# Optimization experiments

Hardware: AMD Instinct MI355X
Metric: run time of the kernel (lower is better)

## Reference

```python
import jax, jax.numpy as jnp
import numpy as np

N_ATOMS = 16384
B_GRAPHS = 64
K_CLUSTERS = 64          # clusters per molecule
M_CLUSTERS = B_GRAPHS * K_CLUSTERS
HID = 256                # hidden_channels (== node_attr feature dim)
FIL = 256                # num_filters
ECH = 64                 # edge_channels (num gaussians)
L_INT = 6                # num_interactions
CUTOFF = 10.0
LN2 = float(np.log(2.0))


def _ssp(x):
    # ShiftedSoftplus
    return jax.nn.softplus(x) - LN2


def setup_inputs() -> dict:
    key = jax.random.key(0)
    ks = jax.random.split(key, 12)
    pos = jax.random.normal(ks[0], (N_ATOMS, 3), jnp.float32) * 2.0
    node_attr = jax.random.normal(ks[1], (N_ATOMS, HID), jnp.float32)
    atoms_per_cluster = N_ATOMS // M_CLUSTERS
    subgraph_index = (jnp.arange(N_ATOMS) // atoms_per_cluster).astype(jnp.int64)
    batch = (jnp.arange(N_ATOMS) // (N_ATOMS // B_GRAPHS)).astype(jnp.int64)
    s = 0.05
    params = {
        "mlp_w1": jax.random.normal(ks[2], (L_INT, ECH, FIL), jnp.float32) * s,
        "mlp_b1": jnp.zeros((L_INT, FIL), jnp.float32),
        "mlp_w2": jax.random.normal(ks[3], (L_INT, FIL, FIL), jnp.float32) * s,
        "mlp_b2": jnp.zeros((L_INT, FIL), jnp.float32),
        "lin1_w": jax.random.normal(ks[4], (L_INT, HID, FIL), jnp.float32) * s,  # no bias
        "lin2_w": jax.random.normal(ks[5], (L_INT, FIL, HID), jnp.float32) * s,
        "lin2_b": jnp.zeros((L_INT, HID), jnp.float32),
        "lin_w":  jax.random.normal(ks[6], (L_INT, HID, HID), jnp.float32) * s,
        "lin_b":  jnp.zeros((L_INT, HID), jnp.float32),
    }
    return {"pos": pos, "node_attr": node_attr,
            "subgraph_index": subgraph_index, "batch": batch,
            "num_graphs": B_GRAPHS, "clusters_per_graph": K_CLUSTERS, **params}


def _complete_graph_edges(num_graphs, clusters_per_graph):
    # static (numpy) construction of per-molecule complete graph, no self loops
    K = clusters_per_graph
    i = np.arange(K)
    pr, pc = np.meshgrid(i, i, indexing='ij')
    m = pr != pc
    pr, pc = pr[m], pc[m]                       # (K*(K-1),)
    off = np.arange(num_graphs)[:, None] * K    # (B,1)
    row = jnp.asarray((off + pr[None, :]).reshape(-1))
    col = jnp.asarray((off + pc[None, :]).reshape(-1))
    return row, col


def reference(pos, node_attr, subgraph_index, batch, num_graphs, clusters_per_graph,
              mlp_w1, mlp_b1, mlp_w2, mlp_b2, lin1_w, lin2_w, lin2_b, lin_w, lin_b):
    M = num_graphs * clusters_per_graph
    # ---- coarse_grain: scatter-mean atoms into clusters ----
    cnt = jax.ops.segment_sum(jnp.ones((pos.shape[0],), pos.dtype), subgraph_index, num_segments=M)
    cnt = jnp.maximum(cnt, 1.0)[:, None]
    cluster_pos = jax.ops.segment_sum(pos, subgraph_index, num_segments=M) / cnt        # (M,3)
    cluster_attr = jax.ops.segment_sum(node_attr, subgraph_index, num_segments=M) / cnt  # (M,H)

    # ---- complete graph per molecule ----
    row, col = _complete_graph_edges(num_graphs, clusters_per_graph)
    edge_length = jnp.linalg.norm(cluster_pos[row] - cluster_pos[col], axis=1)          # (E,)

    # ---- GaussianSmearing ----
    offset = jnp.linspace(0.0, CUTOFF, ECH)
    coeff = -0.5 / (offset[1] - offset[0]) ** 2
    edge_attr = jnp.exp(coeff * (edge_length[:, None] - offset[None, :]) ** 2)          # (E,ECH)

    # smooth cutoff envelope
    C = 0.5 * (jnp.cos(edge_length * jnp.pi / CUTOFF) + 1.0)
    C = C * (edge_length <= CUTOFF).astype(C.dtype)                                     # (E,)

    # ---- SchNetEncoder (embed_node=False) ----
    h = cluster_attr
    for l in range(L_INT):
        # filter-generating MLP
        W = _ssp(edge_attr @ mlp_w1[l] + mlp_b1[l]) @ mlp_w2[l] + mlp_b2[l]             # (E,F)
        W = W * C[:, None]
        x = h @ lin1_w[l]                                                               # (M,F)
        agg = jax.ops.segment_sum(x[row] * W, col, num_segments=M)                      # (M,F)
        x = agg @ lin2_w[l] + lin2_b[l]                                                 # (M,H)
        x = _ssp(x)
        x = x @ lin_w[l] + lin_b[l]
        h = h + x                                                                       # residual
    return h
```

## Files before the change

### kernel.cpp

```cpp
#include <hip/hip_runtime.h>
#include <cstdint>

#define NATOMS 16384
#define BGRAPH 64
#define KC     64
#define MCL    (BGRAPH*KC)
#define HIDC   256
#define FILC   256
#define ECHC   64
#define LINT   6

#define TGRID  1024
#define TROWS  1088
#define NBP    1056

typedef __bf16 bf16x8 __attribute__((ext_vector_type(8)));
typedef __bf16 bf16x2 __attribute__((ext_vector_type(2)));
typedef float  f32x4  __attribute__((ext_vector_type(4)));
typedef unsigned short u16x8 __attribute__((ext_vector_type(8)));

__device__ __forceinline__ float bf2f(unsigned short u) {
    unsigned int x = ((unsigned int)u) << 16;
    return __builtin_bit_cast(float, x);
}
__device__ __forceinline__ unsigned short f2bf(float f) {
    __bf16 h = (__bf16)f;
    return __builtin_bit_cast(unsigned short, h);
}
__device__ __forceinline__ unsigned int pk2(float a, float b) {
    bf16x2 v = { (__bf16)a, (__bf16)b };
    return __builtin_bit_cast(unsigned int, v);
}
__device__ __forceinline__ float ssp_poly(float x) {
    float u = fminf(x * x, 4.0f);
    float q = u * fmaf(u, fmaf(u, 3.4722222e-4f, -5.2083333e-3f), 0.125f);
    return fmaf(0.5f, x, q);
}
__device__ __forceinline__ float ssp_fast(float x) {
    float m = fmaxf(x, 0.0f);
    float t = __builtin_amdgcn_exp2f(-fabsf(x) * 1.44269504088896341f);
    float l = __builtin_amdgcn_logf(1.0f + t);
    return fmaf(0.69314718055994531f, l, m - 0.69314718055994531f);
}
__device__ __forceinline__ int sw_off(int row, int col) {
    int s = (row + (row >> 3)) & 7;
    return row * 256 + ((((col >> 3) ^ s) << 3) | (col & 7));
}
__device__ __forceinline__ int phi_sw(int row) {
    return ((row & 7) ^ ((row >> 3) & 7)) & 7;
}

#define CGB   1024
#define N_W1  (LINT*16384)
#define N_BIG (LINT*65536)
#define PACK_BLOCKS ((N_W1 + 4*N_BIG + 255)/256)
__global__ void k_prep(const float* __restrict__ pos, const float* __restrict__ attr,
                       const int* __restrict__ subi,
                       float* __restrict__ h, unsigned short* __restrict__ h_bf,
                       float* __restrict__ cpos,
                       const float* __restrict__ w1_src, const float* __restrict__ w2_src,
                       const float* __restrict__ l1_src, const float* __restrict__ l2_src,
                       const float* __restrict__ lw_src,
                       unsigned short* __restrict__ w1p, unsigned short* __restrict__ w2p,
                       unsigned short* __restrict__ l1p, unsigned short* __restrict__ l2p,
                       unsigned short* __restrict__ lwp)
{
    if (blockIdx.x >= CGB) {
        int idx = (blockIdx.x - CGB) * 256 + threadIdx.x;
        if (idx < N_W1) {
            int j = idx & 7, lane = (idx >> 3) & 63, kt = (idx >> 9) & 1;
            int mt = (idx >> 10) & 15, l = idx >> 14;
            int ech = kt*32 + (lane >> 4)*8 + j;
            int f1  = mt*16 + (lane & 15);
            w1p[idx] = f2bf(w1_src[(l*64 + ech)*256 + f1]);
            return;
        }
        int r = idx - N_W1;
        int which = r / N_BIG;
        if (which >= 4) return;
        int e = r - which * N_BIG;
        const float* src = (which == 0) ? w2_src : (which == 1) ? l1_src
                         : (which == 2) ? l2_src : lw_src;
        unsigned short* dst = (which == 0) ? w2p : (which == 1) ? l1p
                            : (which == 2) ? l2p : lwp;
        int n = e % 256;
        int k = (e / 256) % 256;
        int l = e / 65536;
        int nt = n >> 4, kt = k >> 5, q = (k >> 3) & 3, j = k & 7;
        int lane = q*16 + (n & 15);
        dst[l*65536 + ((nt*8 + kt)*64 + lane)*8 + j] = f2bf(src[e]);
        return;
    }
    const int m = blockIdx.x * 4 + (threadIdx.x >> 6);
    const int lane = threadIdx.x & 63;
    const bool is64 = (subi[8] == 1);
    int lo = 0, hi = NATOMS;
    while (lo < hi) { int mid = (lo + hi) >> 1;
        int v = is64 ? subi[2*mid] : subi[mid];
        if (v < m) lo = mid + 1; else hi = mid; }
    int lo2 = lo, hi2 = NATOMS;
    while (lo2 < hi2) { int mid = (lo2 + hi2) >> 1;
        int v = is64 ? subi[2*mid] : subi[mid];
        if (v < m + 1) lo2 = mid + 1; else hi2 = mid; }
    const int cnt2 = lo2 - lo;
    const float inv = 1.0f / (float)(cnt2 > 0 ? cnt2 : 1);

    float4 s = {0.f, 0.f, 0.f, 0.f};
    for (int a = lo; a < lo2; a++) {
        const float4 v = *reinterpret_cast<const float4*>(&attr[a*HIDC + lane*4]);
        s.x += v.x; s.y += v.y; s.z += v.z; s.w += v.w;
    }
    s.x *= inv; s.y *= inv; s.z *= inv; s.w *= inv;
    *reinterpret_cast<float4*>(&h[m*HIDC + lane*4]) = s;
    const int o = m*HIDC + lane*4;
    h_bf[o+0] = f2bf(s.x); h_bf[o+1] = f2bf(s.y);
    h_bf[o+2] = f2bf(s.z); h_bf[o+3] = f2bf(s.w);
    if (lane < 3) {
        float p = 0.f;
        for (int a = lo; a < lo2; a++) p += pos[a*3 + lane];
        cpos[m*3 + lane] = p * inv;
    }
}

#define OSTR 264
__global__ __launch_bounds__(512, 6) void k_tab(
    const unsigned short* __restrict__ w1p_all, const unsigned short* __restrict__ w2p_all,
    const float* __restrict__ b1_all, const float* __restrict__ b2_all,
    unsigned short* __restrict__ table)
{
    __shared__ unsigned short G_s[64 * 256];
    __shared__ unsigned short phi_s[16 * OSTR];
    __shared__ float C_s[64];
    __shared__ float d_s[64];

    const int l  = blockIdx.x / 17;
    const int g0 = (blockIdx.x % 17) * 64;
    const unsigned short* w1p = w1p_all + (size_t)l*16384;
    const unsigned short* w2p = w2p_all + (size_t)l*65536;
    const float* b1 = b1_all + l*256;
    const float* b2 = b2_all + l*256;

    const int t  = threadIdx.x;
    const int w  = t >> 6, lane = t & 63;
    const int quad = lane >> 4, l16 = lane & 15;

    if (t < 64) {
        float d = (float)(g0 + t) * 0.009765625f;
        d_s[t] = d;
        float Cv = 0.5f * (__cosf(d * 0.31415926535897932f) + 1.0f);
        C_s[t] = (d <= 10.0f) ? Cv : 0.0f;
    }
    __syncthreads();

    const float DELTA = 10.0f / 63.0f;
    const float C2 = (-0.5f / (DELTA * DELTA)) * 1.44269504088896341f;
    {
        float d = d_s[lane];
        u16x8 ph;
        #pragma unroll
        for (int j = 0; j < 8; j++) {
            float diff = d - (float)(w*8 + j) * DELTA;
            ph[j] = f2bf(__builtin_amdgcn_exp2f(C2 * diff * diff));
        }
        *reinterpret_cast<u16x8*>(&phi_s[lane*64 + ((w ^ phi_sw(lane)) << 3)]) = ph;
    }
    __syncthreads();

    f32x4 acc1[2][4];
    #pragma unroll
    for (int mt = 0; mt < 2; mt++) {
        const int f1b = (w*2 + mt)*16 + quad*4;
        float4 bq = *reinterpret_cast<const float4*>(&b1[f1b]);
        #pragma unroll
        for (int nt = 0; nt < 4; nt++) {
            acc1[mt][nt][0] = bq.x; acc1[mt][nt][1] = bq.y;
            acc1[mt][nt][2] = bq.z; acc1[mt][nt][3] = bq.w;
        }
    }
    #pragma unroll
    for (int kt = 0; kt < 2; kt++) {
        bf16x8 bfr[4];
        #pragma unroll
        for (int nt = 0; nt < 4; nt++) {
            int row = nt*16 + l16;
            bfr[nt] = *reinterpret_cast<const bf16x8*>(
                &phi_s[row*64 + (((kt*4 + quad) ^ phi_sw(row)) << 3)]);
        }
        #pragma unroll
        for (int mt = 0; mt < 2; mt++) {
            bf16x8 afr = *reinterpret_cast<const bf16x8*>(
                w1p + (((w*2 + mt)*2 + kt)*64 + lane)*8);
            #pragma unroll
            for (int nt = 0; nt < 4; nt++)
                acc1[mt][nt] = __builtin_amdgcn_mfma_f32_16x16x32_bf16(afr, bfr[nt], acc1[mt][nt], 0, 0, 0);
        }
    }

    float Cn[4];
    #pragma unroll
    for (int nt = 0; nt < 4; nt++) Cn[nt] = C_s[nt*16 + l16];

    #pragma unroll
    for (int mt = 0; mt < 2; mt++) {
        const int f1b = (w*2 + mt)*16 + quad*4;
        #pragma unroll
        for (int nt = 0; nt < 4; nt++) {
            float v0 = ssp_poly(acc1[mt][nt][0]) * Cn[nt];
            float v1 = ssp_poly(acc1[mt][nt][1]) * Cn[nt];
            float v2 = ssp_poly(acc1[mt][nt][2]) * Cn[nt];
            float v3 = ssp_poly(acc1[mt][nt][3]) * Cn[nt];
            uint2 pp;
            pp.x = pk2(v0, v1);
            pp.y = pk2(v2, v3);
            int edge = nt*16 + l16;
            int s = (edge + (edge >> 3)) & 7;
            int a = edge*256 + ((((f1b >> 3) ^ s) << 3) | (f1b & 7));
            *reinterpret_cast<uint2*>(&G_s[a]) = pp;
        }
    }
    __syncthreads();

    f32x4 acc2[4][2];
    #pragma unroll
    for (int a = 0; a < 4; a++)
        #pragma unroll
        for (int bb = 0; bb < 2; bb++) acc2[a][bb] = f32x4{0.f,0.f,0.f,0.f};

    #pragma unroll
    for (int kt = 0; kt < 8; kt++) {
        bf16x8 afr[4];
        #pragma unroll
        for (int mt = 0; mt < 4; mt++) {
            int row = mt*16 + l16;
            int s = (row + (row >> 3)) & 7;
            afr[mt] = *reinterpret_cast<const bf16x8*>(&G_s[row*256 + (((kt*4 + quad) ^ s) << 3)]);
        }
        #pragma unroll
        for (int nt = 0; nt < 2; nt++) {
            const int ntg = w*2 + nt;
            bf16x8 bfr = *reinterpret_cast<const bf16x8*>(w2p + ((ntg*8 + kt)*64 + lane)*8);
            #pragma unroll
            for (int mt = 0; mt < 4; mt++)
                acc2[mt][nt] = __builtin_amdgcn_mfma_f32_16x16x32_bf16(afr[mt], bfr, acc2[mt][nt], 0, 0, 0);
        }
    }

    #pragma unroll
    for (int nt = 0; nt < 2; nt++) {
        const int f = (w*2 + nt)*16 + l16;
        const float b2v = b2[f];
        #pragma unroll
        for (int mt = 0; mt < 4; mt++) {
            #pragma unroll
            for (int i = 0; i < 4; i++) {
                int e = mt*16 + quad*4 + i;
                table[((size_t)l*TROWS + g0 + e)*256 + f] =
                    f2bf(fmaf(C_s[e], b2v, acc2[mt][nt][i]));
            }
        }
    }
}

__device__ __forceinline__ void gemm16(const unsigned short* A_s, const unsigned short* Bp,
                                       int w, int lane, f32x4 acc[4])
{
    const int quad = lane >> 4, l16 = lane & 15;
    const int s = (l16 + (l16 >> 3)) & 7;
    #pragma unroll
    for (int nt = 0; nt < 4; nt++) acc[nt] = f32x4{0.f,0.f,0.f,0.f};
    #pragma unroll
    for (int kt = 0; kt < 8; kt++) {
        bf16x8 afr = *reinterpret_cast<const bf16x8*>(&A_s[l16*256 + (((kt*4 + quad) ^ s) << 3)]);
        #pragma unroll
        for (int nt = 0; nt < 4; nt++) {
            bf16x8 bfr = *reinterpret_cast<const bf16x8*>(Bp + (((w*4 + nt)*8 + kt)*64 + lane)*8);
            acc[nt] = __builtin_amdgcn_mfma_f32_16x16x32_bf16(afr, bfr, acc[nt], 0, 0, 0);
        }
    }
}
__device__ __forceinline__ void gemm16w16(const unsigned short* A_s, const unsigned short* Bp,
                                          int w, int lane, f32x4& acc)
{
    const int quad = lane >> 4, l16 = lane & 15;
    const int s = (l16 + (l16 >> 3)) & 7;
    acc = f32x4{0.f,0.f,0.f,0.f};
    #pragma unroll
    for (int kt = 0; kt < 8; kt++) {
        bf16x8 afr = *reinterpret_cast<const bf16x8*>(&A_s[l16*256 + (((kt*4 + quad) ^ s) << 3)]);
        bf16x8 bfr = *reinterpret_cast<const bf16x8*>(Bp + (((w*8 + kt)*64 + lane))*8);
        acc = __builtin_amdgcn_mfma_f32_16x16x32_bf16(afr, bfr, acc, 0, 0, 0);
    }
}

#define PK_TOTAL (LINT*NBP*64)
#define PK_BLOCKS ((PK_TOTAL + 255)/256)
__global__ __launch_bounds__(256) void k_gemm0p(
    const unsigned short* __restrict__ A_bf, const unsigned short* __restrict__ Bp,
    unsigned short* __restrict__ out_bf,
    const unsigned short* __restrict__ table, unsigned short* __restrict__ tbl2)
{
    if (blockIdx.x >= 256) {
        int idx = (blockIdx.x - 256) * 256 + threadIdx.x;
        if (idx >= PK_TOTAL) return;
        int fc2 = idx & 63;
        int qq = idx >> 6;
        int bin = qq % NBP;
        int l = qq / NBP;
        if (bin > TGRID) return;
        const unsigned short* Ts = table + ((size_t)l*TROWS + bin)*256 + fc2*4;
        ushort4 a = *reinterpret_cast<const ushort4*>(Ts);
        ushort4 b = *reinterpret_cast<const ushort4*>(Ts + 256);
        ushort4 d;
        d.x = f2bf(bf2f(b.x) - bf2f(a.x));
        d.y = f2bf(bf2f(b.y) - bf2f(a.y));
        d.z = f2bf(bf2f(b.z) - bf2f(a.z));
        d.w = f2bf(bf2f(b.w) - bf2f(a.w));
        unsigned short* dst = tbl2 + ((size_t)l*NBP + bin)*512 + fc2*8;
        *reinterpret_cast<ushort4*>(dst)     = a;
        *reinterpret_cast<ushort4*>(dst + 4) = d;
        return;
    }
    __shared__ unsigned short A_s[16 * 256];
    const int mb = blockIdx.x;
    const int t = threadIdx.x;
    const int w = t >> 6, lane = t & 63, quad = lane >> 4, l16 = lane & 15;

    {
        int r = t >> 4, seg = t & 15;
        int s = (r + (r >> 3)) & 7;
        const u16x8* src = reinterpret_cast<const u16x8*>(A_bf + (size_t)(mb*16 + r)*256 + seg*16);
        int c = seg*2;
        *reinterpret_cast<u16x8*>(&A_s[r*256 + (((c  ) ^ s) << 3)]) = src[0];
        *reinterpret_cast<u16x8*>(&A_s[r*256 + (((c+1) ^ s) << 3)]) = src[1];
    }
    __syncthreads();

    f32x4 acc[4];
    gemm16(A_s, Bp, w, lane, acc);

    #pragma unroll
    for (int nt = 0; nt < 4; nt++)
        #pragma unroll
        for (int i = 0; i < 4; i++) {
            int rg = mb*16 + quad*4 + i;
            int col = w*64 + nt*16 + l16;
            out_bf[(size_t)rg*256 + col] = f2bf(acc[nt][i]);
        }
}

template<int DO_X>
__global__ __launch_bounds__(1024) void k_layer(
    const float* __restrict__ cpos,
    const unsigned short* __restrict__ xin, unsigned short* __restrict__ xout,
    const unsigned short* __restrict__ Tp,
    const unsigned short* __restrict__ lin2p, const float* __restrict__ lin2_b,
    const unsigned short* __restrict__ linp,  const float* __restrict__ lin_b,
    const unsigned short* __restrict__ lin1p,
    float* __restrict__ h)
{
    __shared__ unsigned short x_s[64 * 256];
    __shared__ unsigned short A0[16 * 256];
    __shared__ unsigned short A1[16 * 256];
    __shared__ int   idx_s[1024];
    __shared__ float frac_s[1024];

    const int blk = blockIdx.x;
    const int b = blk >> 2, q = blk & 3;
    const int t = threadIdx.x;
    const int w = t >> 6, lane = t & 63, quad = lane >> 4, l16 = lane & 15;

    {
        int r = t >> 4, seg = t & 15;
        const u16x8* s8 = reinterpret_cast<const u16x8*>(
            xin + ((size_t)(b*64 + r))*256 + seg*16);
        u16x8* dst = reinterpret_cast<u16x8*>(&x_s[r*256 + seg*16]);
        dst[0] = s8[0]; dst[1] = s8[1];
    }
    {
        int r = t >> 4, cc = t & 15;
        int gr = b*64 + r, gc = b*64 + q*16 + cc;
        float ax = cpos[gr*3 + 0] - cpos[gc*3 + 0];
        float ay = cpos[gr*3 + 1] - cpos[gc*3 + 1];
        float az = cpos[gr*3 + 2] - cpos[gc*3 + 2];
        float d = sqrtf(ax*ax + ay*ay + az*az);
        int i; float fr;
        if (gr == gc || d >= 10.0f) { i = TGRID; fr = 0.0f; }
        else {
            float u = d * 102.4f;
            i = (int)u; fr = u - (float)i;
        }
        idx_s[t] = i * 512; frac_s[t] = fr;
    }
    __syncthreads();

    {
        const int c   = t >> 6;
        const int fc2 = t & 63;
        float a4[4] = {0.f, 0.f, 0.f, 0.f};
        #pragma unroll 8
        for (int r = 0; r < 64; r++) {
            const int   pi = __builtin_amdgcn_readfirstlane(idx_s[r*16 + c]);
            const float fr = frac_s[r*16 + c];
            const u16x8 td = *reinterpret_cast<const u16x8*>(Tp + pi + fc2*8);
            const ushort4 x4 = *reinterpret_cast<const ushort4*>(&x_s[r*256 + fc2*4]);
            float w0 = fmaf(fr, bf2f(td[4]), bf2f(td[0]));
            float w1 = fmaf(fr, bf2f(td[5]), bf2f(td[1]));
            float w2 = fmaf(fr, bf2f(td[6]), bf2f(td[2]));
            float w3 = fmaf(fr, bf2f(td[7]), bf2f(td[3]));
            a4[0] = fmaf(bf2f(x4.x), w0, a4[0]);
            a4[1] = fmaf(bf2f(x4.y), w1, a4[1]);
            a4[2] = fmaf(bf2f(x4.z), w2, a4[2]);
            a4[3] = fmaf(bf2f(x4.w), w3, a4[3]);
        }
        uint2 pv;
        pv.x = pk2(a4[0], a4[1]);
        pv.y = pk2(a4[2], a4[3]);
        int s2 = (c + (c >> 3)) & 7;
        *reinterpret_cast<uint2*>(
            &A0[c*256 + ((((fc2 >> 1) ^ s2) << 3) | ((fc2 & 1) * 4))]) = pv;
    }
    __syncthreads();

    const int col = w*16 + l16;
    const int rbase_g = b*64 + q*16;
    f32x4 acc;
    gemm16w16(A0, lin2p, w, lane, acc);
    float bv = lin2_b[col];
    #pragma unroll
    for (int i = 0; i < 4; i++)
        A1[sw_off(quad*4 + i, col)] = f2bf(ssp_fast(acc[i] + bv));
    __syncthreads();

    gemm16w16(A1, linp, w, lane, acc);
    bv = lin_b[col];
    float hv[4];
    #pragma unroll
    for (int i = 0; i < 4; i++) {
        int rg = rbase_g + quad*4 + i;
        float v = acc[i] + bv + h[(size_t)rg*256 + col];
        h[(size_t)rg*256 + col] = v;
        hv[i] = v;
    }
    if (DO_X) {
        #pragma unroll
        for (int i = 0; i < 4; i++)
            A0[sw_off(quad*4 + i, col)] = f2bf(hv[i]);
        __syncthreads();
        gemm16w16(A0, lin1p, w, lane, acc);
        #pragma unroll
        for (int i = 0; i < 4; i++) {
            int rg = rbase_g + quad*4 + i;
            xout[(size_t)rg*256 + col] = f2bf(acc[i]);
        }
    }
}

extern "C" void kernel_launch(void* const* d_in, const int* in_sizes, int n_in,
                              void* d_out, int out_size, void* d_ws, size_t ws_size,
                              hipStream_t stream)
{
    const float* pos    = (const float*)d_in[0];
    const float* nattr  = (const float*)d_in[1];
    const int*   subi   = (const int*)d_in[2];
    const float* mlp_w1 = (const float*)d_in[6];
    const float* mlp_b1 = (const float*)d_in[7];
    const float* mlp_w2 = (const float*)d_in[8];
    const float* mlp_b2 = (const float*)d_in[9];
    const float* lin1_w = (const float*)d_in[10];
    const float* lin2_w = (const float*)d_in[11];
    const float* lin2_b = (const float*)d_in[12];
    const float* lin_w  = (const float*)d_in[13];
    const float* lin_b  = (const float*)d_in[14];
    float* h = (float*)d_out;

    char* p = (char*)d_ws;
    auto alloc = [&](size_t bytes) { char* r = p; p += (bytes + 255) & ~(size_t)255; return r; };
    unsigned short* h_bf   = (unsigned short*)alloc((size_t)MCL*256*2);
    unsigned short* x0buf  = (unsigned short*)alloc((size_t)MCL*256*2);
    unsigned short* x1buf  = (unsigned short*)alloc((size_t)MCL*256*2);
    unsigned short* table  = (unsigned short*)alloc((size_t)LINT*TROWS*256*2);
    unsigned short* tbl2   = (unsigned short*)alloc((size_t)LINT*NBP*512*2);
    float*          cpos   = (float*)alloc((size_t)MCL*3*4);
    unsigned short* w1p    = (unsigned short*)alloc((size_t)LINT*16384*2);
    unsigned short* w2p    = (unsigned short*)alloc((size_t)LINT*65536*2);
    unsigned short* lin1p  = (unsigned short*)alloc((size_t)LINT*65536*2);
    unsigned short* lin2p  = (unsigned short*)alloc((size_t)LINT*65536*2);
    unsigned short* linp   = (unsigned short*)alloc((size_t)LINT*65536*2);

    k_prep<<<CGB + PACK_BLOCKS, 256, 0, stream>>>(
        pos, nattr, subi, h, h_bf, cpos,
        mlp_w1, mlp_w2, lin1_w, lin2_w, lin_w,
        w1p, w2p, lin1p, lin2p, linp);

    k_tab<<<LINT*17, 512, 0, stream>>>(w1p, w2p, mlp_b1, mlp_b2, table);

    k_gemm0p<<<256 + PK_BLOCKS, 256, 0, stream>>>(h_bf, lin1p, x0buf, table, tbl2);

    for (int l = 0; l < LINT; l++) {
        const unsigned short* xin  = (l & 1) ? x1buf : x0buf;
        unsigned short*       xout = (l & 1) ? x0buf : x1buf;
        const unsigned short* Tl = tbl2 + (size_t)l*NBP*512;
        if (l < LINT-1) {
            k_layer<1><<<BGRAPH*4, 1024, 0, stream>>>(cpos, xin, xout, Tl,
                lin2p + (size_t)l*65536, lin2_b + l*256,
                linp + (size_t)l*65536, lin_b + l*256,
                lin1p + (size_t)(l+1)*65536, h);
        } else {
            k_layer<0><<<BGRAPH*4, 1024, 0, stream>>>(cpos, xin, xout, Tl,
                lin2p + (size_t)l*65536, lin2_b + l*256,
                linp + (size_t)l*65536, lin_b + l*256,
                lin1p, h);
        }
    }
}
```

Measured before the change: 231.7 us.

## Fuse table packing and initial GEMM into k_tab; split layers into 512 blocks

The table kernel now writes the interpolation table directly in the paired layout (value plus next-bin value), and the initial lin1 GEMM runs as extra blocks of the same launch, which removes the k_gemm0p kernel and the intermediate table buffer. Each layer kernel now uses 512 blocks of 512 threads covering 8 destination clusters each, instead of 256 blocks of 1024 threads covering 16. The MFMA tiles are padded with zero rows and half of each 16-row tile is discarded, so matrix work per output row doubles in exchange for more blocks and higher occupancy. Interpolation now computes the difference on the fly from two stored values rather than reading a precomputed delta.

```diff
diff --git a/kernel.cpp b/kernel.cpp
--- a/kernel.cpp
+++ b/kernel.cpp
@@ -11,8 +11,7 @@
 #define LINT   6
 
 #define TGRID  1024
-#define TROWS  1088
-#define NBP    1056
+#define NBP    1088
 
 typedef __bf16 bf16x8 __attribute__((ext_vector_type(8)));
 typedef __bf16 bf16x2 __attribute__((ext_vector_type(2)));
@@ -122,16 +121,63 @@
     }
 }
 
-#define OSTR 264
-__global__ __launch_bounds__(512, 6) void k_tab(
+__device__ __forceinline__ void gemm16x2(const unsigned short* A_s, const unsigned short* Bp,
+                                         int w, int lane, f32x4 acc[2])
+{
+    const int quad = lane >> 4, l16 = lane & 15;
+    const int s = (l16 + (l16 >> 3)) & 7;
+    acc[0] = f32x4{0.f,0.f,0.f,0.f};
+    acc[1] = f32x4{0.f,0.f,0.f,0.f};
+    #pragma unroll
+    for (int kt = 0; kt < 8; kt++) {
+        bf16x8 afr = *reinterpret_cast<const bf16x8*>(&A_s[l16*256 + (((kt*4 + quad) ^ s) << 3)]);
+        #pragma unroll
+        for (int nt = 0; nt < 2; nt++) {
+            bf16x8 bfr = *reinterpret_cast<const bf16x8*>(Bp + (((w*2 + nt)*8 + kt)*64 + lane)*8);
+            acc[nt] = __builtin_amdgcn_mfma_f32_16x16x32_bf16(afr, bfr, acc[nt], 0, 0, 0);
+        }
+    }
+}
+
+#define NTB   (LINT*17)
+#define OSTR  264
+__global__ __launch_bounds__(512) void k_tab(
     const unsigned short* __restrict__ w1p_all, const unsigned short* __restrict__ w2p_all,
     const float* __restrict__ b1_all, const float* __restrict__ b2_all,
-    unsigned short* __restrict__ table)
+    unsigned short* __restrict__ tbl2,
+    const unsigned short* __restrict__ h_bf, const unsigned short* __restrict__ lin1p,
+    unsigned short* __restrict__ x0buf)
 {
     __shared__ unsigned short G_s[64 * 256];
     __shared__ unsigned short phi_s[16 * OSTR];
     __shared__ float C_s[64];
     __shared__ float d_s[64];
+
+    const int t  = threadIdx.x;
+    const int w  = t >> 6, lane = t & 63;
+    const int quad = lane >> 4, l16 = lane & 15;
+
+    if (blockIdx.x >= NTB) {
+        const int mb = blockIdx.x - NTB;
+        unsigned short* A_s = G_s;
+        {
+            int r = t >> 5, seg = t & 31;
+            int s = (r + (r >> 3)) & 7;
+            u16x8 v = *reinterpret_cast<const u16x8*>(h_bf + (size_t)(mb*16 + r)*256 + seg*8);
+            *reinterpret_cast<u16x8*>(&A_s[r*256 + ((seg ^ s) << 3)]) = v;
+        }
+        __syncthreads();
+        f32x4 acc[2];
+        gemm16x2(A_s, lin1p, w, lane, acc);
+        #pragma unroll
+        for (int nt = 0; nt < 2; nt++) {
+            int col = (w*2 + nt)*16 + l16;
+            #pragma unroll
+            for (int i = 0; i < 4; i++)
+                x0buf[(size_t)(mb*16 + quad*4 + i)*256 + col] = f2bf(acc[nt][i]);
+        }
+        return;
+    }
 
     const int l  = blockIdx.x / 17;
     const int g0 = (blockIdx.x % 17) * 64;
@@ -139,10 +185,6 @@
     const unsigned short* w2p = w2p_all + (size_t)l*65536;
     const float* b1 = b1_all + l*256;
     const float* b2 = b2_all + l*256;
-
-    const int t  = threadIdx.x;
-    const int w  = t >> 6, lane = t & 63;
-    const int quad = lane >> 4, l16 = lane & 15;
 
     if (t < 64) {
         float d = (float)(g0 + t) * 0.009765625f;
@@ -245,111 +287,29 @@
         }
     }
 
+    unsigned short* base = tbl2 + (size_t)l*NBP*512;
     #pragma unroll
     for (int nt = 0; nt < 2; nt++) {
         const int f = (w*2 + nt)*16 + l16;
         const float b2v = b2[f];
+        const int fc2 = f >> 2, fj = f & 3;
         #pragma unroll
         for (int mt = 0; mt < 4; mt++) {
             #pragma unroll
             for (int i = 0; i < 4; i++) {
                 int e = mt*16 + quad*4 + i;
-                table[((size_t)l*TROWS + g0 + e)*256 + f] =
-                    f2bf(fmaf(C_s[e], b2v, acc2[mt][nt][i]));
+                int bin = g0 + e;
+                unsigned short v = f2bf(fmaf(C_s[e], b2v, acc2[mt][nt][i]));
+                base[(size_t)bin*512 + fc2*8 + fj] = v;
+                if (bin > 0)
+                    base[(size_t)(bin-1)*512 + fc2*8 + 4 + fj] = v;
             }
         }
     }
 }
 
-__device__ __forceinline__ void gemm16(const unsigned short* A_s, const unsigned short* Bp,
-                                       int w, int lane, f32x4 acc[4])
-{
-    const int quad = lane >> 4, l16 = lane & 15;
-    const int s = (l16 + (l16 >> 3)) & 7;
-    #pragma unroll
-    for (int nt = 0; nt < 4; nt++) acc[nt] = f32x4{0.f,0.f,0.f,0.f};
-    #pragma unroll
-    for (int kt = 0; kt < 8; kt++) {
-        bf16x8 afr = *reinterpret_cast<const bf16x8*>(&A_s[l16*256 + (((kt*4 + quad) ^ s) << 3)]);
-        #pragma unroll
-        for (int nt = 0; nt < 4; nt++) {
-            bf16x8 bfr = *reinterpret_cast<const bf16x8*>(Bp + (((w*4 + nt)*8 + kt)*64 + lane)*8);
-            acc[nt] = __builtin_amdgcn_mfma_f32_16x16x32_bf16(afr, bfr, acc[nt], 0, 0, 0);
-        }
-    }
-}
-__device__ __forceinline__ void gemm16w16(const unsigned short* A_s, const unsigned short* Bp,
-                                          int w, int lane, f32x4& acc)
-{
-    const int quad = lane >> 4, l16 = lane & 15;
-    const int s = (l16 + (l16 >> 3)) & 7;
-    acc = f32x4{0.f,0.f,0.f,0.f};
-    #pragma unroll
-    for (int kt = 0; kt < 8; kt++) {
-        bf16x8 afr = *reinterpret_cast<const bf16x8*>(&A_s[l16*256 + (((kt*4 + quad) ^ s) << 3)]);
-        bf16x8 bfr = *reinterpret_cast<const bf16x8*>(Bp + (((w*8 + kt)*64 + lane))*8);
-        acc = __builtin_amdgcn_mfma_f32_16x16x32_bf16(afr, bfr, acc, 0, 0, 0);
-    }
-}
-
-#define PK_TOTAL (LINT*NBP*64)
-#define PK_BLOCKS ((PK_TOTAL + 255)/256)
-__global__ __launch_bounds__(256) void k_gemm0p(
-    const unsigned short* __restrict__ A_bf, const unsigned short* __restrict__ Bp,
-    unsigned short* __restrict__ out_bf,
-    const unsigned short* __restrict__ table, unsigned short* __restrict__ tbl2)
-{
-    if (blockIdx.x >= 256) {
-        int idx = (blockIdx.x - 256) * 256 + threadIdx.x;
-        if (idx >= PK_TOTAL) return;
-        int fc2 = idx & 63;
-        int qq = idx >> 6;
-        int bin = qq % NBP;
-        int l = qq / NBP;
-        if (bin > TGRID) return;
-        const unsigned short* Ts = table + ((size_t)l*TROWS + bin)*256 + fc2*4;
-        ushort4 a = *reinterpret_cast<const ushort4*>(Ts);
-        ushort4 b = *reinterpret_cast<const ushort4*>(Ts + 256);
-        ushort4 d;
-        d.x = f2bf(bf2f(b.x) - bf2f(a.x));
-        d.y = f2bf(bf2f(b.y) - bf2f(a.y));
-        d.z = f2bf(bf2f(b.z) - bf2f(a.z));
-        d.w = f2bf(bf2f(b.w) - bf2f(a.w));
-        unsigned short* dst = tbl2 + ((size_t)l*NBP + bin)*512 + fc2*8;
-        *reinterpret_cast<ushort4*>(dst)     = a;
-        *reinterpret_cast<ushort4*>(dst + 4) = d;
-        return;
-    }
-    __shared__ unsigned short A_s[16 * 256];
-    const int mb = blockIdx.x;
-    const int t = threadIdx.x;
-    const int w = t >> 6, lane = t & 63, quad = lane >> 4, l16 = lane & 15;
-
-    {
-        int r = t >> 4, seg = t & 15;
-        int s = (r + (r >> 3)) & 7;
-        const u16x8* src = reinterpret_cast<const u16x8*>(A_bf + (size_t)(mb*16 + r)*256 + seg*16);
-        int c = seg*2;
-        *reinterpret_cast<u16x8*>(&A_s[r*256 + (((c  ) ^ s) << 3)]) = src[0];
-        *reinterpret_cast<u16x8*>(&A_s[r*256 + (((c+1) ^ s) << 3)]) = src[1];
-    }
-    __syncthreads();
-
-    f32x4 acc[4];
-    gemm16(A_s, Bp, w, lane, acc);
-
-    #pragma unroll
-    for (int nt = 0; nt < 4; nt++)
-        #pragma unroll
-        for (int i = 0; i < 4; i++) {
-            int rg = mb*16 + quad*4 + i;
-            int col = w*64 + nt*16 + l16;
-            out_bf[(size_t)rg*256 + col] = f2bf(acc[nt][i]);
-        }
-}
-
 template<int DO_X>
-__global__ __launch_bounds__(1024) void k_layer(
+__global__ __launch_bounds__(512, 4) void k_layer(
     const float* __restrict__ cpos,
     const unsigned short* __restrict__ xin, unsigned short* __restrict__ xout,
     const unsigned short* __restrict__ Tp,
@@ -361,24 +321,23 @@
     __shared__ unsigned short x_s[64 * 256];
     __shared__ unsigned short A0[16 * 256];
     __shared__ unsigned short A1[16 * 256];
-    __shared__ int   idx_s[1024];
-    __shared__ float frac_s[1024];
-
-    const int blk = blockIdx.x;
-    const int b = blk >> 2, q = blk & 3;
-    const int t = threadIdx.x;
-    const int w = t >> 6, lane = t & 63, quad = lane >> 4, l16 = lane & 15;
+    __shared__ int   idx_s[512];
+    __shared__ float frac_s[512];
+
+    const int b  = blockIdx.x >> 3, e8 = blockIdx.x & 7;
+    const int t  = threadIdx.x;
+    const int w  = t >> 6, lane = t & 63, quad = lane >> 4, l16 = lane & 15;
 
     {
-        int r = t >> 4, seg = t & 15;
+        int r = t >> 3, seg = t & 7;
         const u16x8* s8 = reinterpret_cast<const u16x8*>(
-            xin + ((size_t)(b*64 + r))*256 + seg*16);
-        u16x8* dst = reinterpret_cast<u16x8*>(&x_s[r*256 + seg*16]);
-        dst[0] = s8[0]; dst[1] = s8[1];
+            xin + ((size_t)(b*64 + r))*256 + seg*32);
+        u16x8* dst = reinterpret_cast<u16x8*>(&x_s[r*256 + seg*32]);
+        dst[0] = s8[0]; dst[1] = s8[1]; dst[2] = s8[2]; dst[3] = s8[3];
     }
     {
-        int r = t >> 4, cc = t & 15;
-        int gr = b*64 + r, gc = b*64 + q*16 + cc;
+        int r = t >> 3, cc = t & 7;
+        int gr = b*64 + r, gc = b*64 + e8*8 + cc;
         float ax = cpos[gr*3 + 0] - cpos[gc*3 + 0];
         float ay = cpos[gr*3 + 1] - cpos[gc*3 + 1];
         float az = cpos[gr*3 + 2] - cpos[gc*3 + 2];
@@ -390,6 +349,10 @@
             i = (int)u; fr = u - (float)i;
         }
         idx_s[t] = i * 512; frac_s[t] = fr;
+        if (t < 256) {
+            u16x8 z = {0,0,0,0,0,0,0,0};
+            *reinterpret_cast<u16x8*>(&A0[(8 + (t >> 5))*256 + (t & 31)*8]) = z;
+        }
     }
     __syncthreads();
 
@@ -399,14 +362,16 @@
         float a4[4] = {0.f, 0.f, 0.f, 0.f};
         #pragma unroll 8
         for (int r = 0; r < 64; r++) {
-            const int   pi = __builtin_amdgcn_readfirstlane(idx_s[r*16 + c]);
-            const float fr = frac_s[r*16 + c];
+            const int   pi = __builtin_amdgcn_readfirstlane(idx_s[r*8 + c]);
+            const float fr = frac_s[r*8 + c];
             const u16x8 td = *reinterpret_cast<const u16x8*>(Tp + pi + fc2*8);
             const ushort4 x4 = *reinterpret_cast<const ushort4*>(&x_s[r*256 + fc2*4]);
-            float w0 = fmaf(fr, bf2f(td[4]), bf2f(td[0]));
-            float w1 = fmaf(fr, bf2f(td[5]), bf2f(td[1]));
-            float w2 = fmaf(fr, bf2f(td[6]), bf2f(td[2]));
-            float w3 = fmaf(fr, bf2f(td[7]), bf2f(td[3]));
+            float t0 = bf2f(td[0]), t1 = bf2f(td[1]);
+            float t2 = bf2f(td[2]), t3 = bf2f(td[3]);
+            float w0 = fmaf(fr, bf2f(td[4]) - t0, t0);
+            float w1 = fmaf(fr, bf2f(td[5]) - t1, t1);
+            float w2 = fmaf(fr, bf2f(td[6]) - t2, t2);
+            float w3 = fmaf(fr, bf2f(td[7]) - t3, t3);
             a4[0] = fmaf(bf2f(x4.x), w0, a4[0]);
             a4[1] = fmaf(bf2f(x4.y), w1, a4[1]);
             a4[2] = fmaf(bf2f(x4.z), w2, a4[2]);
@@ -415,42 +380,60 @@
         uint2 pv;
         pv.x = pk2(a4[0], a4[1]);
         pv.y = pk2(a4[2], a4[3]);
-        int s2 = (c + (c >> 3)) & 7;
         *reinterpret_cast<uint2*>(
-            &A0[c*256 + ((((fc2 >> 1) ^ s2) << 3) | ((fc2 & 1) * 4))]) = pv;
-    }
-    __syncthreads();
-
-    const int col = w*16 + l16;
-    const int rbase_g = b*64 + q*16;
-    f32x4 acc;
-    gemm16w16(A0, lin2p, w, lane, acc);
-    float bv = lin2_b[col];
-    #pragma unroll
-    for (int i = 0; i < 4; i++)
-        A1[sw_off(quad*4 + i, col)] = f2bf(ssp_fast(acc[i] + bv));
-    __syncthreads();
-
-    gemm16w16(A1, linp, w, lane, acc);
-    bv = lin_b[col];
-    float hv[4];
-    #pragma unroll
-    for (int i = 0; i < 4; i++) {
-        int rg = rbase_g + quad*4 + i;
-        float v = acc[i] + bv + h[(size_t)rg*256 + col];
-        h[(size_t)rg*256 + col] = v;
-        hv[i] = v;
+            &A0[c*256 + ((((fc2 >> 1) ^ c) << 3) | ((fc2 & 1) * 4))]) = pv;
+    }
+    __syncthreads();
+
+    const int rbase_g = b*64 + e8*8;
+    f32x4 acc[2];
+    gemm16x2(A0, lin2p, w, lane, acc);
+    #pragma unroll
+    for (int nt = 0; nt < 2; nt++) {
+        const int col = (w*2 + nt)*16 + l16;
+        const float bv = lin2_b[col];
+        #pragma unroll
+        for (int i = 0; i < 4; i++)
+            A1[sw_off(quad*4 + i, col)] = f2bf(ssp_fast(acc[nt][i] + bv));
+    }
+    __syncthreads();
+
+    gemm16x2(A1, linp, w, lane, acc);
+    float hv[2][4];
+    if (quad < 2) {
+        #pragma unroll
+        for (int nt = 0; nt < 2; nt++) {
+            const int col = (w*2 + nt)*16 + l16;
+            const float bv = lin_b[col];
+            #pragma unroll
+            for (int i = 0; i < 4; i++) {
+                int rg = rbase_g + quad*4 + i;
+                float v = acc[nt][i] + bv + h[(size_t)rg*256 + col];
+                h[(size_t)rg*256 + col] = v;
+                hv[nt][i] = v;
+            }
+        }
     }
     if (DO_X) {
-        #pragma unroll
-        for (int i = 0; i < 4; i++)
-            A0[sw_off(quad*4 + i, col)] = f2bf(hv[i]);
+        if (quad < 2) {
+            #pragma unroll
+            for (int nt = 0; nt < 2; nt++) {
+                const int col = (w*2 + nt)*16 + l16;
+                #pragma unroll
+                for (int i = 0; i < 4; i++)
+                    A0[sw_off(quad*4 + i, col)] = f2bf(hv[nt][i]);
+            }
+        }
         __syncthreads();
-        gemm16w16(A0, lin1p, w, lane, acc);
-        #pragma unroll
-        for (int i = 0; i < 4; i++) {
-            int rg = rbase_g + quad*4 + i;
-            xout[(size_t)rg*256 + col] = f2bf(acc[i]);
+        gemm16x2(A0, lin1p, w, lane, acc);
+        if (quad < 2) {
+            #pragma unroll
+            for (int nt = 0; nt < 2; nt++) {
+                const int col = (w*2 + nt)*16 + l16;
+                #pragma unroll
+                for (int i = 0; i < 4; i++)
+                    xout[(size_t)(rbase_g + quad*4 + i)*256 + col] = f2bf(acc[nt][i]);
+            }
         }
     }
 }
@@ -478,7 +461,6 @@
     unsigned short* h_bf   = (unsigned short*)alloc((size_t)MCL*256*2);
     unsigned short* x0buf  = (unsigned short*)alloc((size_t)MCL*256*2);
     unsigned short* x1buf  = (unsigned short*)alloc((size_t)MCL*256*2);
-    unsigned short* table  = (unsigned short*)alloc((size_t)LINT*TROWS*256*2);
     unsigned short* tbl2   = (unsigned short*)alloc((size_t)LINT*NBP*512*2);
     float*          cpos   = (float*)alloc((size_t)MCL*3*4);
     unsigned short* w1p    = (unsigned short*)alloc((size_t)LINT*16384*2);
@@ -492,21 +474,20 @@
         mlp_w1, mlp_w2, lin1_w, lin2_w, lin_w,
         w1p, w2p, lin1p, lin2p, linp);
 
-    k_tab<<<LINT*17, 512, 0, stream>>>(w1p, w2p, mlp_b1, mlp_b2, table);
-
-    k_gemm0p<<<256 + PK_BLOCKS, 256, 0, stream>>>(h_bf, lin1p, x0buf, table, tbl2);
+    k_tab<<<NTB + 256, 512, 0, stream>>>(w1p, w2p, mlp_b1, mlp_b2, tbl2,
+                                         h_bf, lin1p, x0buf);
 
     for (int l = 0; l < LINT; l++) {
         const unsigned short* xin  = (l & 1) ? x1buf : x0buf;
         unsigned short*       xout = (l & 1) ? x0buf : x1buf;
         const unsigned short* Tl = tbl2 + (size_t)l*NBP*512;
         if (l < LINT-1) {
-            k_layer<1><<<BGRAPH*4, 1024, 0, stream>>>(cpos, xin, xout, Tl,
+            k_layer<1><<<BGRAPH*8, 512, 0, stream>>>(cpos, xin, xout, Tl,
                 lin2p + (size_t)l*65536, lin2_b + l*256,
                 linp + (size_t)l*65536, lin_b + l*256,
                 lin1p + (size_t)(l+1)*65536, h);
         } else {
-            k_layer<0><<<BGRAPH*4, 1024, 0, stream>>>(cpos, xin, xout, Tl,
+            k_layer<0><<<BGRAPH*8, 512, 0, stream>>>(cpos, xin, xout, Tl,
                 lin2p + (size_t)l*65536, lin2_b + l*256,
                 linp + (size_t)l*65536, lin_b + l*256,
                 lin1p, h);
```

Measured after the change: 252.1 us. 8.8% more time.

## Use nearest-bin filter table at double resolution and fold gemm0 into table kernel

Applied to the files above, without the earlier changes.

The filter-weight lookup table switches from linear interpolation on a 1024-bin grid to nearest-neighbour lookup on a 2048-bin grid. This removes the separate packing pass that built the interleaved value/delta table, the per-edge fraction storage, and the interpolation FMAs in the aggregation loop. Each lookup now reads 8 bytes instead of 16. The initial lin1 GEMM is merged into the table-building launch as extra blocks, which removes one kernel launch. Table generation work doubles, and nearest-bin rounding adds approximation error compared with interpolation.

```diff
diff --git a/kernel.cpp b/kernel.cpp
--- a/kernel.cpp
+++ b/kernel.cpp
@@ -10,9 +10,8 @@
 #define ECHC   64
 #define LINT   6
 
-#define TGRID  1024
-#define TROWS  1088
-#define NBP    1056
+#define TGRID  2048
+#define NBP    2112
 
 typedef __bf16 bf16x8 __attribute__((ext_vector_type(8)));
 typedef __bf16 bf16x2 __attribute__((ext_vector_type(2)));
@@ -122,30 +121,87 @@
     }
 }
 
-#define OSTR 264
-__global__ __launch_bounds__(512, 6) void k_tab(
+__device__ __forceinline__ void gemm16x2(const unsigned short* A_s, const unsigned short* Bp,
+                                         int w, int lane, f32x4 acc[2])
+{
+    const int quad = lane >> 4, l16 = lane & 15;
+    const int s = (l16 + (l16 >> 3)) & 7;
+    acc[0] = f32x4{0.f,0.f,0.f,0.f};
+    acc[1] = f32x4{0.f,0.f,0.f,0.f};
+    #pragma unroll
+    for (int kt = 0; kt < 8; kt++) {
+        bf16x8 afr = *reinterpret_cast<const bf16x8*>(&A_s[l16*256 + (((kt*4 + quad) ^ s) << 3)]);
+        #pragma unroll
+        for (int nt = 0; nt < 2; nt++) {
+            bf16x8 bfr = *reinterpret_cast<const bf16x8*>(Bp + (((w*2 + nt)*8 + kt)*64 + lane)*8);
+            acc[nt] = __builtin_amdgcn_mfma_f32_16x16x32_bf16(afr, bfr, acc[nt], 0, 0, 0);
+        }
+    }
+}
+
+__device__ __forceinline__ void gemm16w16(const unsigned short* A_s, const unsigned short* Bp,
+                                          int w, int lane, f32x4& acc)
+{
+    const int quad = lane >> 4, l16 = lane & 15;
+    const int s = (l16 + (l16 >> 3)) & 7;
+    acc = f32x4{0.f,0.f,0.f,0.f};
+    #pragma unroll
+    for (int kt = 0; kt < 8; kt++) {
+        bf16x8 afr = *reinterpret_cast<const bf16x8*>(&A_s[l16*256 + (((kt*4 + quad) ^ s) << 3)]);
+        bf16x8 bfr = *reinterpret_cast<const bf16x8*>(Bp + (((w*8 + kt)*64 + lane))*8);
+        acc = __builtin_amdgcn_mfma_f32_16x16x32_bf16(afr, bfr, acc, 0, 0, 0);
+    }
+}
+
+#define NTB   (LINT*33)
+#define OSTR  264
+__global__ __launch_bounds__(512) void k_tab(
     const unsigned short* __restrict__ w1p_all, const unsigned short* __restrict__ w2p_all,
     const float* __restrict__ b1_all, const float* __restrict__ b2_all,
-    unsigned short* __restrict__ table)
+    unsigned short* __restrict__ table,
+    const unsigned short* __restrict__ h_bf, const unsigned short* __restrict__ lin1p,
+    unsigned short* __restrict__ x0buf)
 {
     __shared__ unsigned short G_s[64 * 256];
     __shared__ unsigned short phi_s[16 * OSTR];
     __shared__ float C_s[64];
     __shared__ float d_s[64];
 
-    const int l  = blockIdx.x / 17;
-    const int g0 = (blockIdx.x % 17) * 64;
+    const int t  = threadIdx.x;
+    const int w  = t >> 6, lane = t & 63;
+    const int quad = lane >> 4, l16 = lane & 15;
+
+    if (blockIdx.x >= NTB) {
+        const int mb = blockIdx.x - NTB;
+        unsigned short* A_s = G_s;
+        {
+            int r = t >> 5, seg = t & 31;
+            int s = (r + (r >> 3)) & 7;
+            u16x8 v = *reinterpret_cast<const u16x8*>(h_bf + (size_t)(mb*16 + r)*256 + seg*8);
+            *reinterpret_cast<u16x8*>(&A_s[r*256 + ((seg ^ s) << 3)]) = v;
+        }
+        __syncthreads();
+        f32x4 acc[2];
+        gemm16x2(A_s, lin1p, w, lane, acc);
+        #pragma unroll
+        for (int nt = 0; nt < 2; nt++) {
+            int col = (w*2 + nt)*16 + l16;
+            #pragma unroll
+            for (int i = 0; i < 4; i++)
+                x0buf[(size_t)(mb*16 + quad*4 + i)*256 + col] = f2bf(acc[nt][i]);
+        }
+        return;
+    }
+
+    const int l  = blockIdx.x / 33;
+    const int g0 = (blockIdx.x % 33) * 64;
     const unsigned short* w1p = w1p_all + (size_t)l*16384;
     const unsigned short* w2p = w2p_all + (size_t)l*65536;
     const float* b1 = b1_all + l*256;
     const float* b2 = b2_all + l*256;
 
-    const int t  = threadIdx.x;
-    const int w  = t >> 6, lane = t & 63;
-    const int quad = lane >> 4, l16 = lane & 15;
-
     if (t < 64) {
-        float d = (float)(g0 + t) * 0.009765625f;
+        float d = (float)(g0 + t) * 0.0048828125f;
         d_s[t] = d;
         float Cv = 0.5f * (__cosf(d * 0.31415926535897932f) + 1.0f);
         C_s[t] = (d <= 10.0f) ? Cv : 0.0f;
@@ -245,6 +301,7 @@
         }
     }
 
+    unsigned short* base = table + (size_t)l*NBP*256;
     #pragma unroll
     for (int nt = 0; nt < 2; nt++) {
         const int f = (w*2 + nt)*16 + l16;
@@ -254,98 +311,11 @@
             #pragma unroll
             for (int i = 0; i < 4; i++) {
                 int e = mt*16 + quad*4 + i;
-                table[((size_t)l*TROWS + g0 + e)*256 + f] =
+                base[(size_t)(g0 + e)*256 + f] =
                     f2bf(fmaf(C_s[e], b2v, acc2[mt][nt][i]));
             }
         }
     }
-}
-
-__device__ __forceinline__ void gemm16(const unsigned short* A_s, const unsigned short* Bp,
-                                       int w, int lane, f32x4 acc[4])
-{
-    const int quad = lane >> 4, l16 = lane & 15;
-    const int s = (l16 + (l16 >> 3)) & 7;
-    #pragma unroll
-    for (int nt = 0; nt < 4; nt++) acc[nt] = f32x4{0.f,0.f,0.f,0.f};
-    #pragma unroll
-    for (int kt = 0; kt < 8; kt++) {
-        bf16x8 afr = *reinterpret_cast<const bf16x8*>(&A_s[l16*256 + (((kt*4 + quad) ^ s) << 3)]);
-        #pragma unroll
-        for (int nt = 0; nt < 4; nt++) {
-            bf16x8 bfr = *reinterpret_cast<const bf16x8*>(Bp + (((w*4 + nt)*8 + kt)*64 + lane)*8);
-            acc[nt] = __builtin_amdgcn_mfma_f32_16x16x32_bf16(afr, bfr, acc[nt], 0, 0, 0);
-        }
-    }
-}
-__device__ __forceinline__ void gemm16w16(const unsigned short* A_s, const unsigned short* Bp,
-                                          int w, int lane, f32x4& acc)
-{
-    const int quad = lane >> 4, l16 = lane & 15;
-    const int s = (l16 + (l16 >> 3)) & 7;
-    acc = f32x4{0.f,0.f,0.f,0.f};
-    #pragma unroll
-    for (int kt = 0; kt < 8; kt++) {
-        bf16x8 afr = *reinterpret_cast<const bf16x8*>(&A_s[l16*256 + (((kt*4 + quad) ^ s) << 3)]);
-        bf16x8 bfr = *reinterpret_cast<const bf16x8*>(Bp + (((w*8 + kt)*64 + lane))*8);
-        acc = __builtin_amdgcn_mfma_f32_16x16x32_bf16(afr, bfr, acc, 0, 0, 0);
-    }
-}
-
-#define PK_TOTAL (LINT*NBP*64)
-#define PK_BLOCKS ((PK_TOTAL + 255)/256)
-__global__ __launch_bounds__(256) void k_gemm0p(
-    const unsigned short* __restrict__ A_bf, const unsigned short* __restrict__ Bp,
-    unsigned short* __restrict__ out_bf,
-    const unsigned short* __restrict__ table, unsigned short* __restrict__ tbl2)
-{
-    if (blockIdx.x >= 256) {
-        int idx = (blockIdx.x - 256) * 256 + threadIdx.x;
-        if (idx >= PK_TOTAL) return;
-        int fc2 = idx & 63;
-        int qq = idx >> 6;
-        int bin = qq % NBP;
-        int l = qq / NBP;
-        if (bin > TGRID) return;
-        const unsigned short* Ts = table + ((size_t)l*TROWS + bin)*256 + fc2*4;
-        ushort4 a = *reinterpret_cast<const ushort4*>(Ts);
-        ushort4 b = *reinterpret_cast<const ushort4*>(Ts + 256);
-        ushort4 d;
-        d.x = f2bf(bf2f(b.x) - bf2f(a.x));
-        d.y = f2bf(bf2f(b.y) - bf2f(a.y));
-        d.z = f2bf(bf2f(b.z) - bf2f(a.z));
-        d.w = f2bf(bf2f(b.w) - bf2f(a.w));
-        unsigned short* dst = tbl2 + ((size_t)l*NBP + bin)*512 + fc2*8;
-        *reinterpret_cast<ushort4*>(dst)     = a;
-        *reinterpret_cast<ushort4*>(dst + 4) = d;
-        return;
-    }
-    __shared__ unsigned short A_s[16 * 256];
-    const int mb = blockIdx.x;
-    const int t = threadIdx.x;
-    const int w = t >> 6, lane = t & 63, quad = lane >> 4, l16 = lane & 15;
-
-    {
-        int r = t >> 4, seg = t & 15;
-        int s = (r + (r >> 3)) & 7;
-        const u16x8* src = reinterpret_cast<const u16x8*>(A_bf + (size_t)(mb*16 + r)*256 + seg*16);
-        int c = seg*2;
-        *reinterpret_cast<u16x8*>(&A_s[r*256 + (((c  ) ^ s) << 3)]) = src[0];
-        *reinterpret_cast<u16x8*>(&A_s[r*256 + (((c+1) ^ s) << 3)]) = src[1];
-    }
-    __syncthreads();
-
-    f32x4 acc[4];
-    gemm16(A_s, Bp, w, lane, acc);
-
-    #pragma unroll
-    for (int nt = 0; nt < 4; nt++)
-        #pragma unroll
-        for (int i = 0; i < 4; i++) {
-            int rg = mb*16 + quad*4 + i;
-            int col = w*64 + nt*16 + l16;
-            out_bf[(size_t)rg*256 + col] = f2bf(acc[nt][i]);
-        }
 }
 
 template<int DO_X>
@@ -361,8 +331,7 @@
     __shared__ unsigned short x_s[64 * 256];
     __shared__ unsigned short A0[16 * 256];
     __shared__ unsigned short A1[16 * 256];
-    __shared__ int   idx_s[1024];
-    __shared__ float frac_s[1024];
+    __shared__ int idx_s[1024];
 
     const int blk = blockIdx.x;
     const int b = blk >> 2, q = blk & 3;
@@ -383,13 +352,13 @@
         float ay = cpos[gr*3 + 1] - cpos[gc*3 + 1];
         float az = cpos[gr*3 + 2] - cpos[gc*3 + 2];
         float d = sqrtf(ax*ax + ay*ay + az*az);
-        int i; float fr;
-        if (gr == gc || d >= 10.0f) { i = TGRID; fr = 0.0f; }
+        int i;
+        if (gr == gc || d >= 10.0f) i = TGRID;
         else {
-            float u = d * 102.4f;
-            i = (int)u; fr = u - (float)i;
-        }
-        idx_s[t] = i * 512; frac_s[t] = fr;
+            i = (int)fmaf(d, 204.8f, 0.5f);
+            if (i > TGRID) i = TGRID;
+        }
+        idx_s[t] = i * 256;
     }
     __syncthreads();
 
@@ -399,18 +368,13 @@
         float a4[4] = {0.f, 0.f, 0.f, 0.f};
         #pragma unroll 8
         for (int r = 0; r < 64; r++) {
-            const int   pi = __builtin_amdgcn_readfirstlane(idx_s[r*16 + c]);
-            const float fr = frac_s[r*16 + c];
-            const u16x8 td = *reinterpret_cast<const u16x8*>(Tp + pi + fc2*8);
+            const int pi = __builtin_amdgcn_readfirstlane(idx_s[r*16 + c]);
+            const ushort4 t4 = *reinterpret_cast<const ushort4*>(Tp + pi + fc2*4);
             const ushort4 x4 = *reinterpret_cast<const ushort4*>(&x_s[r*256 + fc2*4]);
-            float w0 = fmaf(fr, bf2f(td[4]), bf2f(td[0]));
-            float w1 = fmaf(fr, bf2f(td[5]), bf2f(td[1]));
-            float w2 = fmaf(fr, bf2f(td[6]), bf2f(td[2]));
-            float w3 = fmaf(fr, bf2f(td[7]), bf2f(td[3]));
-            a4[0] = fmaf(bf2f(x4.x), w0, a4[0]);
-            a4[1] = fmaf(bf2f(x4.y), w1, a4[1]);
-            a4[2] = fmaf(bf2f(x4.z), w2, a4[2]);
-            a4[3] = fmaf(bf2f(x4.w), w3, a4[3]);
+            a4[0] = fmaf(bf2f(x4.x), bf2f(t4.x), a4[0]);
+            a4[1] = fmaf(bf2f(x4.y), bf2f(t4.y), a4[1]);
+            a4[2] = fmaf(bf2f(x4.z), bf2f(t4.z), a4[2]);
+            a4[3] = fmaf(bf2f(x4.w), bf2f(t4.w), a4[3]);
         }
         uint2 pv;
         pv.x = pk2(a4[0], a4[1]);
@@ -478,8 +442,7 @@
     unsigned short* h_bf   = (unsigned short*)alloc((size_t)MCL*256*2);
     unsigned short* x0buf  = (unsigned short*)alloc((size_t)MCL*256*2);
     unsigned short* x1buf  = (unsigned short*)alloc((size_t)MCL*256*2);
-    unsigned short* table  = (unsigned short*)alloc((size_t)LINT*TROWS*256*2);
-    unsigned short* tbl2   = (unsigned short*)alloc((size_t)LINT*NBP*512*2);
+    unsigned short* table  = (unsigned short*)alloc((size_t)LINT*NBP*256*2);
     float*          cpos   = (float*)alloc((size_t)MCL*3*4);
     unsigned short* w1p    = (unsigned short*)alloc((size_t)LINT*16384*2);
     unsigned short* w2p    = (unsigned short*)alloc((size_t)LINT*65536*2);
@@ -492,14 +455,13 @@
         mlp_w1, mlp_w2, lin1_w, lin2_w, lin_w,
         w1p, w2p, lin1p, lin2p, linp);
 
-    k_tab<<<LINT*17, 512, 0, stream>>>(w1p, w2p, mlp_b1, mlp_b2, table);
-
-    k_gemm0p<<<256 + PK_BLOCKS, 256, 0, stream>>>(h_bf, lin1p, x0buf, table, tbl2);
+    k_tab<<<NTB + 256, 512, 0, stream>>>(w1p, w2p, mlp_b1, mlp_b2, table,
+                                         h_bf, lin1p, x0buf);
 
     for (int l = 0; l < LINT; l++) {
         const unsigned short* xin  = (l & 1) ? x1buf : x0buf;
         unsigned short*       xout = (l & 1) ? x0buf : x1buf;
-        const unsigned short* Tl = tbl2 + (size_t)l*NBP*512;
+        const unsigned short* Tl = table + (size_t)l*NBP*256;
         if (l < LINT-1) {
             k_layer<1><<<BGRAPH*4, 1024, 0, stream>>>(cpos, xin, xout, Tl,
                 lin2p + (size_t)l*65536, lin2_b + l*256,
```

Measured after the change: 213.7 us. 1.08x faster.
